# Kernel tuning notes

Hardware: AMD Instinct MI355X
Metric: run time of the kernel (lower is better)

The kernel has to match this reference:

```python
import jax, jax.numpy as jnp
import numpy as np

EPS = 1e-5
N, DEG, D, L = 50000, 16, 128, 2  # nodes, max_neighbor, embed_size, gnn_layer


def _log_map_zero(y):
    # Poincare ball log map at origin: atanh(||y||) * y / ||y||, with clamps
    n = jnp.linalg.norm(y, axis=-1, keepdims=True)
    nc = jnp.clip(n, EPS, 1.0 - EPS)
    return y * (jnp.arctanh(nc) / nc)


def _exp_map_zero(v):
    # Poincare ball exp map at origin: tanh(||v||) * v / ||v||
    n = jnp.linalg.norm(v, axis=-1, keepdims=True)
    nc = jnp.maximum(n, EPS)
    return v * (jnp.tanh(nc) / nc)


def setup_inputs() -> dict:
    key = jax.random.key(0)
    k1, k2, k3, k4, k5 = jax.random.split(key, 5)
    node_repr = jax.random.normal(k1, (N, D), jnp.float32) * 0.1
    adj = jax.random.randint(k2, (N, DEG), 0, N)
    weight = jax.random.normal(k3, (N, DEG), jnp.float32)
    mask = jnp.ones((N, 1), jnp.float32)
    # per-relation, per-layer message weights (2 relations: pos / neg edges)
    scale = 1.0 / np.sqrt(D)
    W_pos = jax.random.normal(k4, (L, D, D), jnp.float32) * scale
    W_neg = jax.random.normal(k5, (L, D, D), jnp.float32) * scale
    return {"node_repr": node_repr, "adj": adj, "weight": weight,
            "mask": mask, "W_pos": W_pos, "W_neg": W_neg}


def reference(node_repr, adj, weight, mask, W_pos, W_neg):
    # split_graph_by_negative_edge
    pos_m = (weight > 0).astype(weight.dtype)
    neg_m = (weight < 0).astype(weight.dtype)
    adjs = (adj * pos_m.astype(adj.dtype), adj * neg_m.astype(adj.dtype))
    ws = (weight * pos_m, (-weight) * neg_m)
    Ws = (W_pos, W_neg)

    x = node_repr
    for step in range(L):
        x = (_log_map_zero(x) if step > 0 else x) * mask
        combined = jnp.zeros_like(x)
        for a, w, W in zip(adjs, ws, Ws):
            msg = (x @ W[step]) * mask                    # [N, D]
            nb = msg[a.reshape(-1)].reshape(N, DEG, D)    # neighbor gather
            combined = combined + jnp.sum(w[..., None] * nb, axis=1)
        combined = combined * mask                        # dropout identity (eval)
        x = _exp_map_zero(combined) * mask
        x = jax.nn.relu(x) * mask                         # poincare activation
    return x
```

## Files before the change

### kernel.cpp

```cpp
#include <hip/hip_runtime.h>
#include <math.h>

#define DD 128
#define DEG 16
#define NPW 16
#define LDST 136
#define EPSV 1e-5f

typedef _Float16 half4_t __attribute__((ext_vector_type(4)));
typedef _Float16 half8_t __attribute__((ext_vector_type(8)));
typedef float    f32x4   __attribute__((ext_vector_type(4)));

__global__ void prep(const float* __restrict__ x, const float* __restrict__ mask,
                     _Float16* __restrict__ x16, int n4, int xb,
                     const float* __restrict__ Wp, const float* __restrict__ Wn,
                     _Float16* __restrict__ WT)
{
    if ((int)blockIdx.x < xb) {
        int i = blockIdx.x * blockDim.x + threadIdx.x;
        if (i >= n4) return;
        float m = mask[i >> 5];
        float m2 = m * m;
        float4 v = ((const float4*)x)[i];
        half4_t h;
        h[0] = (_Float16)(v.x * m2); h[1] = (_Float16)(v.y * m2);
        h[2] = (_Float16)(v.z * m2); h[3] = (_Float16)(v.w * m2);
        ((half4_t*)x16)[i] = h;
    } else {
        int bid   = blockIdx.x - xb;
        int mat   = bid >> 3;
        int chunk = bid & 7;
        int l = mat >> 1, rel = mat & 1;
        const float* __restrict__ src = (rel ? Wn : Wp) + (size_t)l * DD * DD;
        _Float16* __restrict__ dst = WT + (size_t)mat * DD * DD;
        for (int o = chunk * 2048 + threadIdx.x; o < chunk * 2048 + 2048; o += 256) {
            int nn = o >> 7, kk = o & 127;
            dst[o] = (_Float16)src[kk * DD + nn];
        }
    }
}

__global__ __launch_bounds__(256, 4) void fused_layer(
    const _Float16* __restrict__ src16,
    const int*   __restrict__ adj, const float* __restrict__ wgt,
    const float* __restrict__ mask,
    const _Float16* __restrict__ WTp, const _Float16* __restrict__ WTn,
    float* __restrict__ dst_f32, _Float16* __restrict__ dst_f16,
    int n, int apply_logmap)
{
    __shared__ __align__(16) _Float16 aggP[4][NPW][LDST];
    __shared__ __align__(16) _Float16 aggN[4][NPW][LDST];

    const int tid    = threadIdx.x;
    const int wv     = tid >> 6;
    const int l64    = tid & 63;
    const int hw     = l64 >> 5;
    const int lane32 = l64 & 31;

    const int wave_id = blockIdx.x * 4 + wv;
    const int row0    = wave_id * NPW;
    if (row0 >= n) return;

    _Float16 (* __restrict__ aP_lds)[LDST] = aggP[wv];
    _Float16 (* __restrict__ aN_lds)[LDST] = aggN[wv];

    for (int i = 0; i < 8; ++i) {
        const int r    = hw * 8 + i;
        const int node = row0 + r;
        float aP[4] = {0.f, 0.f, 0.f, 0.f};
        float aN[4] = {0.f, 0.f, 0.f, 0.f};
        if (node < n) {
            const int*   __restrict__ arow = adj + (size_t)node * DEG;
            const float* __restrict__ wrow = wgt + (size_t)node * DEG;
            int4   ia0 = ((const int4*)arow)[0];
            int4   ia1 = ((const int4*)arow)[1];
            int4   ia2 = ((const int4*)arow)[2];
            int4   ia3 = ((const int4*)arow)[3];
            float4 wa0 = ((const float4*)wrow)[0];
            float4 wa1 = ((const float4*)wrow)[1];
            float4 wa2 = ((const float4*)wrow)[2];
            float4 wa3 = ((const float4*)wrow)[3];
            const int idxs[16] = {ia0.x, ia0.y, ia0.z, ia0.w, ia1.x, ia1.y, ia1.z, ia1.w,
                                  ia2.x, ia2.y, ia2.z, ia2.w, ia3.x, ia3.y, ia3.z, ia3.w};
            const float ws[16] = {wa0.x, wa0.y, wa0.z, wa0.w, wa1.x, wa1.y, wa1.z, wa1.w,
                                  wa2.x, wa2.y, wa2.z, wa2.w, wa3.x, wa3.y, wa3.z, wa3.w};
            half4_t v[16];
            #pragma unroll
            for (int j = 0; j < 16; ++j)
                v[j] = *(const half4_t*)(src16 + (size_t)idxs[j] * DD + lane32 * 4);
            #pragma unroll
            for (int j = 0; j < 16; ++j) {
                float wp = fmaxf(ws[j], 0.f);
                float wn = fmaxf(-ws[j], 0.f);
                #pragma unroll
                for (int c = 0; c < 4; ++c) {
                    float f = (float)v[j][c];
                    aP[c] += wp * f;
                    aN[c] += wn * f;
                }
            }
        }
        half4_t hP, hN;
        #pragma unroll
        for (int c = 0; c < 4; ++c) { hP[c] = (_Float16)aP[c]; hN[c] = (_Float16)aN[c]; }
        *(half4_t*)&aP_lds[r][lane32 * 4] = hP;
        *(half4_t*)&aN_lds[r][lane32 * 4] = hN;
    }
    __threadfence_block();

    const int l15  = l64 & 15;
    const int quad = l64 >> 4;

    half8_t aPf[4], aNf[4];
    #pragma unroll
    for (int kb = 0; kb < 4; ++kb) {
        aPf[kb] = *(const half8_t*)&aP_lds[l15][kb * 32 + quad * 8];
        aNf[kb] = *(const half8_t*)&aN_lds[l15][kb * 32 + quad * 8];
    }

    f32x4 acc[8];
    #pragma unroll
    for (int nb = 0; nb < 8; ++nb) acc[nb] = (f32x4){0.f, 0.f, 0.f, 0.f};
    #pragma unroll
    for (int nb = 0; nb < 8; ++nb) {
        const _Float16* bp = WTp + (size_t)(nb * 16 + l15) * DD + quad * 8;
        const _Float16* bn = WTn + (size_t)(nb * 16 + l15) * DD + quad * 8;
        #pragma unroll
        for (int kb = 0; kb < 4; ++kb) {
            acc[nb] = __builtin_amdgcn_mfma_f32_16x16x32_f16(
                aPf[kb], *(const half8_t*)(bp + kb * 32), acc[nb], 0, 0, 0);
            acc[nb] = __builtin_amdgcn_mfma_f32_16x16x32_f16(
                aNf[kb], *(const half8_t*)(bn + kb * 32), acc[nb], 0, 0, 0);
        }
    }

    #pragma unroll
    for (int r = 0; r < 4; ++r) {
        const int rl  = quad * 4 + r;
        const int row = row0 + rl;
        const float m = (row < n) ? mask[row] : 0.f;

        float cv[8];
        float c2 = 0.f;
        #pragma unroll
        for (int nb = 0; nb < 8; ++nb) { cv[nb] = acc[nb][r] * m; c2 += cv[nb] * cv[nb]; }
        c2 += __shfl_xor(c2, 1); c2 += __shfl_xor(c2, 2);
        c2 += __shfl_xor(c2, 4); c2 += __shfl_xor(c2, 8);
        float nc = fmaxf(sqrtf(c2), EPSV);
        float sc = tanhf(nc) / nc;

        float xv[8];
        float s2 = 0.f;
        #pragma unroll
        for (int nb = 0; nb < 8; ++nb) {
            float t = fmaxf(cv[nb] * sc * m, 0.f) * m;
            xv[nb] = t; s2 += t * t;
        }

        if (apply_logmap) {
            s2 += __shfl_xor(s2, 1); s2 += __shfl_xor(s2, 2);
            s2 += __shfl_xor(s2, 4); s2 += __shfl_xor(s2, 8);
            float nc2 = fminf(fmaxf(sqrtf(s2), EPSV), 1.f - EPSV);
            float f = (atanhf(nc2) / nc2) * m * m;
            if (row < n) {
                _Float16* drow = dst_f16 + (size_t)row * DD + l15;
                #pragma unroll
                for (int nb = 0; nb < 8; ++nb) drow[nb * 16] = (_Float16)(xv[nb] * f);
            }
        } else {
            if (row < n) {
                float* drow = dst_f32 + (size_t)row * DD + l15;
                #pragma unroll
                for (int nb = 0; nb < 8; ++nb) drow[nb * 16] = xv[nb];
            }
        }
    }
}

extern "C" void kernel_launch(void* const* d_in, const int* in_sizes, int n_in,
                              void* d_out, int out_size, void* d_ws, size_t ws_size,
                              hipStream_t stream)
{
    const float* node_repr = (const float*)d_in[0];
    const int*   adj       = (const int*)  d_in[1];
    const float* weight    = (const float*)d_in[2];
    const float* mask      = (const float*)d_in[3];
    const float* W_pos     = (const float*)d_in[4];
    const float* W_neg     = (const float*)d_in[5];

    const int n = in_sizes[0] / DD;

    _Float16* x16 = (_Float16*)d_ws;
    _Float16* y16 = x16 + (size_t)n * DD;
    _Float16* WT  = y16 + (size_t)n * DD;

    const int n4 = n * DD / 4;
    const int xb = (n4 + 255) / 256;
    prep<<<xb + 32, 256, 0, stream>>>(node_repr, mask, x16, n4, xb,
                                      W_pos, W_neg, WT);

    const int waves = (n + NPW - 1) / NPW;
    dim3 grid((waves + 3) / 4);
    fused_layer<<<grid, 256, 0, stream>>>(x16, adj, weight, mask,
                                          WT + 0 * DD * DD, WT + 1 * DD * DD,
                                          nullptr, y16, n, 1);
    fused_layer<<<grid, 256, 0, stream>>>(y16, adj, weight, mask,
                                          WT + 2 * DD * DD, WT + 3 * DD * DD,
                                          (float*)d_out, nullptr, n, 0);
}
```

Measured before the change: 210.1 us.

## Double-buffer neighbor gathers and load adjacency rows once per half-wave via shuffles

Each half-wave now loads its 8 rows of adjacency indices and weights with one coalesced vector load and hands them out to lanes with shuffles, replacing the per-row serial loads. The gather loop is software-pipelined with two register buffers, so the next row's 16 neighbor loads are in flight while the current row is accumulated. Occupancy is lowered to 3 blocks per SM to leave room for the extra registers. The n bounds check inside the gather loop is removed, so the code assumes n is a multiple of 16, which holds for N=50000; otherwise it would read out of bounds.

```diff
diff --git a/kernel.cpp b/kernel.cpp
--- a/kernel.cpp
+++ b/kernel.cpp
@@ -10,6 +10,19 @@
 typedef _Float16 half4_t __attribute__((ext_vector_type(4)));
 typedef _Float16 half8_t __attribute__((ext_vector_type(8)));
 typedef float    f32x4   __attribute__((ext_vector_type(4)));
+
+__device__ __forceinline__ int4 shfl4i(int4 v, int src) {
+    int4 r;
+    r.x = __shfl(v.x, src, 32); r.y = __shfl(v.y, src, 32);
+    r.z = __shfl(v.z, src, 32); r.w = __shfl(v.w, src, 32);
+    return r;
+}
+__device__ __forceinline__ float4 shfl4f(float4 v, int src) {
+    float4 r;
+    r.x = __shfl(v.x, src, 32); r.y = __shfl(v.y, src, 32);
+    r.z = __shfl(v.z, src, 32); r.w = __shfl(v.w, src, 32);
+    return r;
+}
 
 __global__ void prep(const float* __restrict__ x, const float* __restrict__ mask,
                      _Float16* __restrict__ x16, int n4, int xb,
@@ -40,7 +53,7 @@
     }
 }
 
-__global__ __launch_bounds__(256, 4) void fused_layer(
+__global__ __launch_bounds__(256, 3) void fused_layer(
     const _Float16* __restrict__ src16,
     const int*   __restrict__ adj, const float* __restrict__ wgt,
     const float* __restrict__ mask,
@@ -64,47 +77,57 @@
     _Float16 (* __restrict__ aP_lds)[LDST] = aggP[wv];
     _Float16 (* __restrict__ aN_lds)[LDST] = aggN[wv];
 
-    for (int i = 0; i < 8; ++i) {
-        const int r    = hw * 8 + i;
-        const int node = row0 + r;
+    const int hrow0 = row0 + hw * 8;
+    int4   mi = ((const int4*)  (adj + (size_t)hrow0 * DEG))[lane32];
+    float4 mw = ((const float4*)(wgt + (size_t)hrow0 * DEG))[lane32];
+
+    auto issue = [&](int i, half4_t* v) {
+        int4 a0 = shfl4i(mi, 4 * i + 0);
+        int4 a1 = shfl4i(mi, 4 * i + 1);
+        int4 a2 = shfl4i(mi, 4 * i + 2);
+        int4 a3 = shfl4i(mi, 4 * i + 3);
+        const int id[16] = {a0.x, a0.y, a0.z, a0.w, a1.x, a1.y, a1.z, a1.w,
+                            a2.x, a2.y, a2.z, a2.w, a3.x, a3.y, a3.z, a3.w};
+        #pragma unroll
+        for (int j = 0; j < 16; ++j)
+            v[j] = *(const half4_t*)(src16 + (size_t)id[j] * DD + lane32 * 4);
+    };
+    auto accum = [&](int i, half4_t* v) {
+        float4 w0 = shfl4f(mw, 4 * i + 0);
+        float4 w1 = shfl4f(mw, 4 * i + 1);
+        float4 w2 = shfl4f(mw, 4 * i + 2);
+        float4 w3 = shfl4f(mw, 4 * i + 3);
+        const float ww[16] = {w0.x, w0.y, w0.z, w0.w, w1.x, w1.y, w1.z, w1.w,
+                              w2.x, w2.y, w2.z, w2.w, w3.x, w3.y, w3.z, w3.w};
         float aP[4] = {0.f, 0.f, 0.f, 0.f};
         float aN[4] = {0.f, 0.f, 0.f, 0.f};
-        if (node < n) {
-            const int*   __restrict__ arow = adj + (size_t)node * DEG;
-            const float* __restrict__ wrow = wgt + (size_t)node * DEG;
-            int4   ia0 = ((const int4*)arow)[0];
-            int4   ia1 = ((const int4*)arow)[1];
-            int4   ia2 = ((const int4*)arow)[2];
-            int4   ia3 = ((const int4*)arow)[3];
-            float4 wa0 = ((const float4*)wrow)[0];
-            float4 wa1 = ((const float4*)wrow)[1];
-            float4 wa2 = ((const float4*)wrow)[2];
-            float4 wa3 = ((const float4*)wrow)[3];
-            const int idxs[16] = {ia0.x, ia0.y, ia0.z, ia0.w, ia1.x, ia1.y, ia1.z, ia1.w,
-                                  ia2.x, ia2.y, ia2.z, ia2.w, ia3.x, ia3.y, ia3.z, ia3.w};
-            const float ws[16] = {wa0.x, wa0.y, wa0.z, wa0.w, wa1.x, wa1.y, wa1.z, wa1.w,
-                                  wa2.x, wa2.y, wa2.z, wa2.w, wa3.x, wa3.y, wa3.z, wa3.w};
-            half4_t v[16];
+        #pragma unroll
+        for (int j = 0; j < 16; ++j) {
+            float wp = fmaxf(ww[j], 0.f);
+            float wn = fmaxf(-ww[j], 0.f);
             #pragma unroll
-            for (int j = 0; j < 16; ++j)
-                v[j] = *(const half4_t*)(src16 + (size_t)idxs[j] * DD + lane32 * 4);
-            #pragma unroll
-            for (int j = 0; j < 16; ++j) {
-                float wp = fmaxf(ws[j], 0.f);
-                float wn = fmaxf(-ws[j], 0.f);
-                #pragma unroll
-                for (int c = 0; c < 4; ++c) {
-                    float f = (float)v[j][c];
-                    aP[c] += wp * f;
-                    aN[c] += wn * f;
-                }
+            for (int c = 0; c < 4; ++c) {
+                float f = (float)v[j][c];
+                aP[c] += wp * f;
+                aN[c] += wn * f;
             }
         }
+        const int r = hw * 8 + i;
         half4_t hP, hN;
         #pragma unroll
         for (int c = 0; c < 4; ++c) { hP[c] = (_Float16)aP[c]; hN[c] = (_Float16)aN[c]; }
         *(half4_t*)&aP_lds[r][lane32 * 4] = hP;
         *(half4_t*)&aN_lds[r][lane32 * 4] = hN;
+    };
+
+    half4_t va[16], vb[16];
+    issue(0, va);
+    #pragma unroll
+    for (int i = 0; i < 8; i += 2) {
+        if (i + 1 < 8) issue(i + 1, vb);
+        accum(i, va);
+        if (i + 2 < 8) issue(i + 2, va);
+        accum(i + 1, vb);
     }
     __threadfence_block();
 
```

Measured after the change: 200.0 us. -4.8%, faster.
